# Kernel optimization log

Hardware: AMD Instinct MI355X
Metric: run time of the kernel (lower is better)

Reference implementation:

```python
import jax, jax.numpy as jnp
import numpy as np

TD_MAX = 1024  # matches init_kwargs td_max; ensemble_average=True


def setup_inputs() -> dict:
    key = jax.random.key(0)
    # trajectory: [T_frames, N_particles, 3]
    x = jax.random.normal(key, (4096, 2048, 3), dtype=jnp.float32)
    return {"x": x}


def reference(x):
    # Original (ensemble_average=True):
    #   MSD[td] = (1/n_t0) * sum_{t0=0}^{n_t0-1} mean_{n,d} (x[t0+td] - x[t0])^2
    # Since every t0 window has the same (N,3) size, this equals a single
    # mean over (t0, n, d) per lag td. We scan over lags to avoid
    # materializing the full [td_max, n_t0, N, 3] gather.
    T = x.shape[0]
    n_t0 = T - TD_MAX
    base = x[:n_t0]  # [n_t0, N, 3] shared origin frames

    def per_lag(carry, td):
        win = jax.lax.dynamic_slice_in_dim(x, td, n_t0, axis=0)  # [n_t0, N, 3]
        d = win - base
        return carry, jnp.mean(d * d)

    _, msd = jax.lax.scan(per_lag, None, jnp.arange(TD_MAX))
    return msd  # [td_max]
```

## Files before the change

kernel.cpp:

```cpp
#include <hip/hip_runtime.h>
#include <stdint.h>

#define T_TOTAL 4096
#define NT0     3072
#define CH      6144
#define TD_MAXL 1024

#define KS     4
#define KC     (CH / KS)
#define BK     32
#define NSTEP  (KC / BK)
#define NTI    24
#define ND     9
#define NTILE  (NTI * ND)
#define NBLK   (NTILE * KS)
#define LDHF   40

typedef _Float16 half8 __attribute__((ext_vector_type(8)));
typedef float    f32x4 __attribute__((ext_vector_type(4)));


__device__ inline void gload16(const void* g, void* l) {
    __builtin_amdgcn_global_load_lds(
        (const __attribute__((address_space(1))) unsigned int*)g,
        (__attribute__((address_space(3))) unsigned int*)l, 16, 0, 0);
}

__global__ __launch_bounds__(256) void s_kernel(const float* __restrict__ x,
                                                float* __restrict__ S,
                                                float* __restrict__ C) {
    const int t = blockIdx.x;
    if (t < TD_MAXL && threadIdx.x == 0) C[t] = 0.0f;
    const float4* row = (const float4*)(x + (size_t)t * CH);
    float s = 0.f;
    for (int k = threadIdx.x; k < CH / 4; k += 256) {
        float4 v = row[k];
        s = fmaf(v.x, v.x, s); s = fmaf(v.y, v.y, s);
        s = fmaf(v.z, v.z, s); s = fmaf(v.w, v.w, s);
    }
    #pragma unroll
    for (int off = 32; off >= 1; off >>= 1) s += __shfl_xor(s, off, 64);
    __shared__ float part[4];
    const int lane = threadIdx.x & 63, wid = threadIdx.x >> 6;
    if (lane == 0) part[wid] = s;
    __syncthreads();
    if (threadIdx.x == 0) S[t] = part[0] + part[1] + part[2] + part[3];
}

__device__ inline half8 pack8(const float4 u, const float4 v) {
    half8 h;
    h[0] = (_Float16)u.x; h[1] = (_Float16)u.y; h[2] = (_Float16)u.z; h[3] = (_Float16)u.w;
    h[4] = (_Float16)v.x; h[5] = (_Float16)v.y; h[6] = (_Float16)v.z; h[7] = (_Float16)v.w;
    return h;
}

__global__ __launch_bounds__(256) void cvt_kernel(const float* __restrict__ x,
                                                  _Float16* __restrict__ xh) {
    const size_t total = (size_t)T_TOTAL * CH;
    size_t i = ((size_t)blockIdx.x * 256 + threadIdx.x) * 8;
    const size_t stride = (size_t)gridDim.x * 256 * 8;
    for (; i < total; i += stride) {
        float4 u = *(const float4*)(x + i);
        float4 v = *(const float4*)(x + i + 4);
        *(half8*)(xh + i) = pack8(u, v);
    }
}

__global__ __launch_bounds__(256, 4) void cross_mfma(const _Float16* __restrict__ xh,
                                                     float* __restrict__ C) {
    __shared__ _Float16 As[2][128][BK];
    __shared__ _Float16 Bs[2][128][BK];
    __shared__ float    C_loc[256];

    const int tid = threadIdx.x;
    const int bid = blockIdx.x;
    const int xcd  = bid & 7;
    const int slot = bid >> 3;
    const int ks   = slot / 27;
    const int tt   = slot % 27;
    const int tile = xcd * 27 + tt;
    const int I    = tile / ND;
    const int D    = tile % ND;
    const int i0 = I * 128, j0 = (I + D) * 128;
    const int k0 = ks * KC;

    C_loc[tid] = 0.f;

    const int lane = tid & 63, wid = tid >> 6;

    const int rsub  = lane >> 2;
    const int pslot = lane & 3;
    const int swz   = ((pslot ^ (rsub & 3)) << 3);
    const int c0row = wid * 32;
    const _Float16* sA0 = xh + (size_t)(i0 + c0row + rsub) * CH + k0 + swz;
    const _Float16* sB0 = xh + (size_t)(j0 + c0row + rsub) * CH + k0 + swz;

#define STAGE(buf, toff) { \
        const size_t ko = (size_t)(toff) * BK; \
        gload16(sA0 + ko,            &As[buf][c0row][0]);      \
        gload16(sA0 + 16 * CH + ko,  &As[buf][c0row + 16][0]); \
        gload16(sB0 + ko,            &Bs[buf][c0row][0]);      \
        gload16(sB0 + 16 * CH + ko,  &Bs[buf][c0row + 16][0]); \
    }

    const int wm = wid >> 1, wn = wid & 1;
    const int fr = lane & 15, ss = lane >> 4;
    const int rdslot = ((ss ^ (fr & 3)) << 4);
    const int offA = (wm * 64 + fr) * 64 + rdslot;
    const int offB = (wn * 64 + fr) * 64 + rdslot;

    f32x4 acc[4][4];
    #pragma unroll
    for (int m = 0; m < 4; ++m)
        #pragma unroll
        for (int n = 0; n < 4; ++n) acc[m][n] = (f32x4)0.f;

    STAGE(0, 0);
    __syncthreads();

    int cur = 0;
    for (int t = 0; t < NSTEP; ++t) {
        if (t + 1 < NSTEP) STAGE(cur ^ 1, t + 1);

        const char* bA = (const char*)&As[cur][0][0];
        const char* bB = (const char*)&Bs[cur][0][0];
        half8 fA[4], fB[4];
        #pragma unroll
        for (int m = 0; m < 4; ++m)
            fA[m] = *(const half8*)(bA + offA + m * (16 * BK * 2));
        #pragma unroll
        for (int n = 0; n < 4; ++n)
            fB[n] = *(const half8*)(bB + offB + n * (16 * BK * 2));
        #pragma unroll
        for (int m = 0; m < 4; ++m)
            #pragma unroll
            for (int n = 0; n < 4; ++n)
                acc[m][n] = __builtin_amdgcn_mfma_f32_16x16x32_f16(fA[m], fB[n],
                                                                   acc[m][n], 0, 0, 0);
        __syncthreads();
        cur ^= 1;
    }
#undef STAGE

    float buck[7][4];
    #pragma unroll
    for (int dd = 0; dd < 7; ++dd)
        #pragma unroll
        for (int rr = 0; rr < 4; ++rr) buck[dd][rr] = 0.f;
    #pragma unroll
    for (int m = 0; m < 4; ++m)
        #pragma unroll
        for (int n = 0; n < 4; ++n)
            #pragma unroll
            for (int rr = 0; rr < 4; ++rr)
                buck[n - m + 3][rr] += acc[m][n][rr];

    const int obase = 64 * (wn - wm) + 128 + (fr - (ss << 2));
    #pragma unroll
    for (int dd = 0; dd < 7; ++dd)
        #pragma unroll
        for (int rr = 0; rr < 4; ++rr)
            atomicAdd(&C_loc[obase + 16 * (dd - 3) - rr], buck[dd][rr]);
    __syncthreads();

    const int td = D * 128 + tid - 128;
    if (td >= 0 && td < TD_MAXL) atomicAdd(&C[td], C_loc[tid]);
}

__global__ __launch_bounds__(256, 2) void cross_fallback(const float* __restrict__ x,
                                                         float* __restrict__ C) {
    __shared__ _Float16 As[2][128][LDHF];
    __shared__ _Float16 Bs[2][128][LDHF];
    __shared__ float    C_loc[256];
    const int tid = threadIdx.x;
    const int bid = blockIdx.x;
    const int xcd  = bid & 7;
    const int slot = bid >> 3;
    const int ks   = slot / 27;
    const int tt   = slot % 27;
    const int tile = xcd * 27 + tt;
    const int I    = tile / ND;
    const int D    = tile % ND;
    const int i0 = I * 128, j0 = (I + D) * 128;
    const int k0 = ks * KC;
    C_loc[tid] = 0.f;
    const int srow = tid >> 1, skq = (tid & 1) << 4;
    const float* gA = x + (size_t)(i0 + srow) * CH + k0 + skq;
    const float* gB = x + (size_t)(j0 + srow) * CH + k0 + skq;
    const int lane = tid & 63, wid = tid >> 6;
    const int wm = wid >> 1, wn = wid & 1;
    const int fr = lane & 15, ss = lane >> 4;
    const int rowA = wm * 64 + fr, rowB = wn * 64 + fr;
    f32x4 acc[4][4];
    #pragma unroll
    for (int m = 0; m < 4; ++m)
        #pragma unroll
        for (int n = 0; n < 4; ++n) acc[m][n] = (f32x4)0.f;
    {
        float4 a[4], b[4];
        #pragma unroll
        for (int q = 0; q < 4; ++q) { a[q] = ((const float4*)gA)[q]; b[q] = ((const float4*)gB)[q]; }
        *(half8*)&As[0][srow][skq]     = pack8(a[0], a[1]);
        *(half8*)&As[0][srow][skq + 8] = pack8(a[2], a[3]);
        *(half8*)&Bs[0][srow][skq]     = pack8(b[0], b[1]);
        *(half8*)&Bs[0][srow][skq + 8] = pack8(b[2], b[3]);
    }
    int cur = 0;
    for (int t = 0; t < NSTEP; ++t) {
        __syncthreads();
        float4 a[4], b[4];
        const bool more = (t + 1 < NSTEP);
        if (more) {
            const float* pA = gA + (size_t)(t + 1) * BK;
            const float* pB = gB + (size_t)(t + 1) * BK;
            #pragma unroll
            for (int q = 0; q < 4; ++q) { a[q] = ((const float4*)pA)[q]; b[q] = ((const float4*)pB)[q]; }
        }
        half8 fA[4], fB[4];
        #pragma unroll
        for (int m = 0; m < 4; ++m) fA[m] = *(const half8*)&As[cur][rowA + 16 * m][ss * 8];
        #pragma unroll
        for (int n = 0; n < 4; ++n) fB[n] = *(const half8*)&Bs[cur][rowB + 16 * n][ss * 8];
        #pragma unroll
        for (int m = 0; m < 4; ++m)
            #pragma unroll
            for (int n = 0; n < 4; ++n)
                acc[m][n] = __builtin_amdgcn_mfma_f32_16x16x32_f16(fA[m], fB[n], acc[m][n], 0, 0, 0);
        if (more) {
            const int nb = cur ^ 1;
            *(half8*)&As[nb][srow][skq]     = pack8(a[0], a[1]);
            *(half8*)&As[nb][srow][skq + 8] = pack8(a[2], a[3]);
            *(half8*)&Bs[nb][srow][skq]     = pack8(b[0], b[1]);
            *(half8*)&Bs[nb][srow][skq + 8] = pack8(b[2], b[3]);
        }
        cur ^= 1;
    }
    float buck[7][4];
    #pragma unroll
    for (int dd = 0; dd < 7; ++dd)
        #pragma unroll
        for (int rr = 0; rr < 4; ++rr) buck[dd][rr] = 0.f;
    #pragma unroll
    for (int m = 0; m < 4; ++m)
        #pragma unroll
        for (int n = 0; n < 4; ++n)
            #pragma unroll
            for (int rr = 0; rr < 4; ++rr)
                buck[n - m + 3][rr] += acc[m][n][rr];
    const int obase = 64 * (wn - wm) + 128 + (fr - (ss << 2));
    #pragma unroll
    for (int dd = 0; dd < 7; ++dd)
        #pragma unroll
        for (int rr = 0; rr < 4; ++rr)
            atomicAdd(&C_loc[obase + 16 * (dd - 3) - rr], buck[dd][rr]);
    __syncthreads();
    const int td = D * 128 + tid - 128;
    if (td >= 0 && td < TD_MAXL) atomicAdd(&C[td], C_loc[tid]);
}

__global__ __launch_bounds__(256) void combine_kernel(const float* __restrict__ S,
                                                      const float* __restrict__ C,
                                                      float* __restrict__ out) {
    const int td = blockIdx.x;
    float p = 0.f, q = 0.f;
    for (int t = threadIdx.x; t < NT0; t += 256) {
        p += S[t + td];
        q += S[t];
    }
    #pragma unroll
    for (int off = 32; off >= 1; off >>= 1) {
        p += __shfl_xor(p, off, 64);
        q += __shfl_xor(q, off, 64);
    }
    __shared__ float pp[4], qq[4];
    const int lane = threadIdx.x & 63, wid = threadIdx.x >> 6;
    if (lane == 0) { pp[wid] = p; qq[wid] = q; }
    __syncthreads();
    if (threadIdx.x == 0) {
        const float P = pp[0] + pp[1] + pp[2] + pp[3];
        const float Q = qq[0] + qq[1] + qq[2] + qq[3];
        const float inv_M = 1.0f / ((float)NT0 * (float)CH);
        out[td] = (P + Q - 2.0f * C[td]) * inv_M;
    }
}

extern "C" void kernel_launch(void* const* d_in, const int* in_sizes, int n_in,
                              void* d_out, int out_size, void* d_ws, size_t ws_size,
                              hipStream_t stream) {
    const float* x = (const float*)d_in[0];
    float* out = (float*)d_out;
    float* S = (float*)d_ws;
    float* C = (float*)((char*)d_ws + 16384);
    _Float16* xh = (_Float16*)((char*)d_ws + 32768);
    const size_t need = 32768 + (size_t)T_TOTAL * CH * sizeof(_Float16);

    s_kernel<<<dim3(T_TOTAL), dim3(256), 0, stream>>>(x, S, C);
    if (ws_size >= need) {
        cvt_kernel<<<dim3(12288), dim3(256), 0, stream>>>(x, xh);
        cross_mfma<<<dim3(NBLK), dim3(256), 0, stream>>>(xh, C);
    } else {
        cross_fallback<<<dim3(NBLK), dim3(256), 0, stream>>>(x, C);
    }
    combine_kernel<<<dim3(TD_MAXL), dim3(256), 0, stream>>>(S, C, out);
}
```

Baseline: 261.1 us.

## Fuse norm and fp16 conversion, enlarge cross-correlation tiles to 256x256

Merges the row-norm kernel and the fp16 conversion kernel into one prep kernel, so the fp32 trajectory is read once instead of twice. Replaces the 128x128 MFMA tile with a 256x256 tile using 512 threads, 8x4 accumulators per wave and a split-K of 8, which raises arithmetic intensity per LDS load. The cost is fewer banded tiles, more wasted work past the lag limit, higher register pressure and different occupancy. The fallback path now also runs the prep kernel, which writes to xh even though the workspace was too small.

```diff
diff --git a/kernel.cpp b/kernel.cpp
--- a/kernel.cpp
+++ b/kernel.cpp
@@ -6,14 +6,18 @@
 #define CH      6144
 #define TD_MAXL 1024
 
-#define KS     4
-#define KC     (CH / KS)
+#define KS2    8
+#define KC2    (CH / KS2)
 #define BK     32
-#define NSTEP  (KC / BK)
-#define NTI    24
-#define ND     9
-#define NTILE  (NTI * ND)
-#define NBLK   (NTILE * KS)
+#define NSTEP2 (KC2 / BK)
+#define NI2    12
+#define ND2    5
+#define NBLK2  (NI2 * ND2 * KS2)
+
+#define KSF    4
+#define KCF    (CH / KSF)
+#define NSTEPF (KCF / BK)
+#define NDF    9
 #define LDHF   40
 
 typedef _Float16 half8 __attribute__((ext_vector_type(8)));
@@ -24,27 +28,6 @@
     __builtin_amdgcn_global_load_lds(
         (const __attribute__((address_space(1))) unsigned int*)g,
         (__attribute__((address_space(3))) unsigned int*)l, 16, 0, 0);
-}
-
-__global__ __launch_bounds__(256) void s_kernel(const float* __restrict__ x,
-                                                float* __restrict__ S,
-                                                float* __restrict__ C) {
-    const int t = blockIdx.x;
-    if (t < TD_MAXL && threadIdx.x == 0) C[t] = 0.0f;
-    const float4* row = (const float4*)(x + (size_t)t * CH);
-    float s = 0.f;
-    for (int k = threadIdx.x; k < CH / 4; k += 256) {
-        float4 v = row[k];
-        s = fmaf(v.x, v.x, s); s = fmaf(v.y, v.y, s);
-        s = fmaf(v.z, v.z, s); s = fmaf(v.w, v.w, s);
-    }
-    #pragma unroll
-    for (int off = 32; off >= 1; off >>= 1) s += __shfl_xor(s, off, 64);
-    __shared__ float part[4];
-    const int lane = threadIdx.x & 63, wid = threadIdx.x >> 6;
-    if (lane == 0) part[wid] = s;
-    __syncthreads();
-    if (threadIdx.x == 0) S[t] = part[0] + part[1] + part[2] + part[3];
 }
 
 __device__ inline half8 pack8(const float4 u, const float4 v) {
@@ -54,64 +37,74 @@
     return h;
 }
 
-__global__ __launch_bounds__(256) void cvt_kernel(const float* __restrict__ x,
-                                                  _Float16* __restrict__ xh) {
-    const size_t total = (size_t)T_TOTAL * CH;
-    size_t i = ((size_t)blockIdx.x * 256 + threadIdx.x) * 8;
-    const size_t stride = (size_t)gridDim.x * 256 * 8;
-    for (; i < total; i += stride) {
-        float4 u = *(const float4*)(x + i);
-        float4 v = *(const float4*)(x + i + 4);
-        *(half8*)(xh + i) = pack8(u, v);
-    }
-}
-
-__global__ __launch_bounds__(256, 4) void cross_mfma(const _Float16* __restrict__ xh,
-                                                     float* __restrict__ C) {
-    __shared__ _Float16 As[2][128][BK];
-    __shared__ _Float16 Bs[2][128][BK];
-    __shared__ float    C_loc[256];
+__global__ __launch_bounds__(256) void prep_kernel(const float* __restrict__ x,
+                                                   _Float16* __restrict__ xh,
+                                                   float* __restrict__ S,
+                                                   float* __restrict__ C) {
+    const int t = blockIdx.x;
+    if (t < TD_MAXL && threadIdx.x == 0) C[t] = 0.0f;
+    const float4* row = (const float4*)(x + (size_t)t * CH);
+    _Float16* orow = xh + (size_t)t * CH;
+    float s = 0.f;
+    for (int k = threadIdx.x; k < CH / 8; k += 256) {
+        float4 u = row[2 * k], v = row[2 * k + 1];
+        s = fmaf(u.x, u.x, s); s = fmaf(u.y, u.y, s);
+        s = fmaf(u.z, u.z, s); s = fmaf(u.w, u.w, s);
+        s = fmaf(v.x, v.x, s); s = fmaf(v.y, v.y, s);
+        s = fmaf(v.z, v.z, s); s = fmaf(v.w, v.w, s);
+        *(half8*)(orow + 8 * k) = pack8(u, v);
+    }
+    #pragma unroll
+    for (int off = 32; off >= 1; off >>= 1) s += __shfl_xor(s, off, 64);
+    __shared__ float part[4];
+    const int lane = threadIdx.x & 63, wid = threadIdx.x >> 6;
+    if (lane == 0) part[wid] = s;
+    __syncthreads();
+    if (threadIdx.x == 0) S[t] = part[0] + part[1] + part[2] + part[3];
+}
+
+__global__ __launch_bounds__(512, 2) void cross_mfma2(const _Float16* __restrict__ xh,
+                                                      float* __restrict__ C) {
+    __shared__ _Float16 Ps[2][2][256][BK];
+    __shared__ float    C_loc[512];
 
     const int tid = threadIdx.x;
     const int bid = blockIdx.x;
-    const int xcd  = bid & 7;
+    const int ks   = bid & 7;
     const int slot = bid >> 3;
-    const int ks   = slot / 27;
-    const int tt   = slot % 27;
-    const int tile = xcd * 27 + tt;
-    const int I    = tile / ND;
-    const int D    = tile % ND;
-    const int i0 = I * 128, j0 = (I + D) * 128;
-    const int k0 = ks * KC;
-
-    C_loc[tid] = 0.f;
+    const int I    = slot / ND2;
+    const int D    = slot % ND2;
+    const int i0 = I * 256, j0 = (I + D) * 256;
+    const int k0 = ks * KC2;
+
+    if (tid < 512) C_loc[tid] = 0.f;
 
     const int lane = tid & 63, wid = tid >> 6;
 
-    const int rsub  = lane >> 2;
-    const int pslot = lane & 3;
-    const int swz   = ((pslot ^ (rsub & 3)) << 3);
-    const int c0row = wid * 32;
-    const _Float16* sA0 = xh + (size_t)(i0 + c0row + rsub) * CH + k0 + swz;
-    const _Float16* sB0 = xh + (size_t)(j0 + c0row + rsub) * CH + k0 + swz;
-
-#define STAGE(buf, toff) { \
-        const size_t ko = (size_t)(toff) * BK; \
-        gload16(sA0 + ko,            &As[buf][c0row][0]);      \
-        gload16(sA0 + 16 * CH + ko,  &As[buf][c0row + 16][0]); \
-        gload16(sB0 + ko,            &Bs[buf][c0row][0]);      \
-        gload16(sB0 + 16 * CH + ko,  &Bs[buf][c0row + 16][0]); \
-    }
-
-    const int wm = wid >> 1, wn = wid & 1;
+    const int isB  = wid >> 2;
+    const int wq   = wid & 3;
+    const int rsub = lane >> 2;
+    const int pslot= lane & 3;
+    const int swz  = (pslot ^ (rsub & 3)) << 3;
+    const _Float16* src0 = xh
+        + (size_t)((isB ? j0 : i0) + wq * 64 + rsub) * CH + k0 + swz;
+
+#define STAGE(buf, t) { \
+        gload16(src0 + (size_t)(t) * BK,               &Ps[buf][isB][wq * 64][0]);      \
+        gload16(src0 + (size_t)(t) * BK + 16 * CH,     &Ps[buf][isB][wq * 64 + 16][0]); \
+        gload16(src0 + (size_t)(t) * BK + 32 * CH,     &Ps[buf][isB][wq * 64 + 32][0]); \
+        gload16(src0 + (size_t)(t) * BK + 48 * CH,     &Ps[buf][isB][wq * 64 + 48][0]); \
+    }
+
+    const int wm = wid >> 2, wn = wid & 3;
     const int fr = lane & 15, ss = lane >> 4;
-    const int rdslot = ((ss ^ (fr & 3)) << 4);
-    const int offA = (wm * 64 + fr) * 64 + rdslot;
-    const int offB = (wn * 64 + fr) * 64 + rdslot;
-
-    f32x4 acc[4][4];
-    #pragma unroll
-    for (int m = 0; m < 4; ++m)
+    const int rdslot = (ss ^ (fr & 3)) << 4;
+    const int offA = (wm * 128 + fr) * (BK * 2) + rdslot;
+    const int offB = (wn * 64 + fr) * (BK * 2) + rdslot;
+
+    f32x4 acc[8][4];
+    #pragma unroll
+    for (int m = 0; m < 8; ++m)
         #pragma unroll
         for (int n = 0; n < 4; ++n) acc[m][n] = (f32x4)0.f;
 
@@ -119,20 +112,20 @@
     __syncthreads();
 
     int cur = 0;
-    for (int t = 0; t < NSTEP; ++t) {
-        if (t + 1 < NSTEP) STAGE(cur ^ 1, t + 1);
-
-        const char* bA = (const char*)&As[cur][0][0];
-        const char* bB = (const char*)&Bs[cur][0][0];
-        half8 fA[4], fB[4];
-        #pragma unroll
-        for (int m = 0; m < 4; ++m)
+    for (int t = 0; t < NSTEP2; ++t) {
+        if (t + 1 < NSTEP2) STAGE(cur ^ 1, t + 1);
+
+        const char* bA = (const char*)&Ps[cur][0][0][0];
+        const char* bB = (const char*)&Ps[cur][1][0][0];
+        half8 fA[8], fB[4];
+        #pragma unroll
+        for (int m = 0; m < 8; ++m)
             fA[m] = *(const half8*)(bA + offA + m * (16 * BK * 2));
         #pragma unroll
         for (int n = 0; n < 4; ++n)
             fB[n] = *(const half8*)(bB + offB + n * (16 * BK * 2));
         #pragma unroll
-        for (int m = 0; m < 4; ++m)
+        for (int m = 0; m < 8; ++m)
             #pragma unroll
             for (int n = 0; n < 4; ++n)
                 acc[m][n] = __builtin_amdgcn_mfma_f32_16x16x32_f16(fA[m], fB[n],
@@ -142,29 +135,31 @@
     }
 #undef STAGE
 
-    float buck[7][4];
-    #pragma unroll
-    for (int dd = 0; dd < 7; ++dd)
+    float buck[11][4];
+    #pragma unroll
+    for (int dd = 0; dd < 11; ++dd)
         #pragma unroll
         for (int rr = 0; rr < 4; ++rr) buck[dd][rr] = 0.f;
     #pragma unroll
-    for (int m = 0; m < 4; ++m)
+    for (int m = 0; m < 8; ++m)
         #pragma unroll
         for (int n = 0; n < 4; ++n)
             #pragma unroll
             for (int rr = 0; rr < 4; ++rr)
-                buck[n - m + 3][rr] += acc[m][n][rr];
-
-    const int obase = 64 * (wn - wm) + 128 + (fr - (ss << 2));
-    #pragma unroll
-    for (int dd = 0; dd < 7; ++dd)
+                buck[n - m + 7][rr] += acc[m][n][rr];
+
+    const int obase = 64 * wn - 128 * wm + 255 + (fr - (ss << 2));
+    #pragma unroll
+    for (int dd = 0; dd < 11; ++dd)
         #pragma unroll
         for (int rr = 0; rr < 4; ++rr)
-            atomicAdd(&C_loc[obase + 16 * (dd - 3) - rr], buck[dd][rr]);
-    __syncthreads();
-
-    const int td = D * 128 + tid - 128;
-    if (td >= 0 && td < TD_MAXL) atomicAdd(&C[td], C_loc[tid]);
+            atomicAdd(&C_loc[obase + 16 * (dd - 7) - rr], buck[dd][rr]);
+    __syncthreads();
+
+    if (tid < 511) {
+        const int td = D * 256 + tid - 255;
+        if (td >= 0 && td < TD_MAXL) atomicAdd(&C[td], C_loc[tid]);
+    }
 }
 
 __global__ __launch_bounds__(256, 2) void cross_fallback(const float* __restrict__ x,
@@ -179,10 +174,10 @@
     const int ks   = slot / 27;
     const int tt   = slot % 27;
     const int tile = xcd * 27 + tt;
-    const int I    = tile / ND;
-    const int D    = tile % ND;
+    const int I    = tile / NDF;
+    const int D    = tile % NDF;
     const int i0 = I * 128, j0 = (I + D) * 128;
-    const int k0 = ks * KC;
+    const int k0 = ks * KCF;
     C_loc[tid] = 0.f;
     const int srow = tid >> 1, skq = (tid & 1) << 4;
     const float* gA = x + (size_t)(i0 + srow) * CH + k0 + skq;
@@ -206,10 +201,10 @@
         *(half8*)&Bs[0][srow][skq + 8] = pack8(b[2], b[3]);
     }
     int cur = 0;
-    for (int t = 0; t < NSTEP; ++t) {
+    for (int t = 0; t < NSTEPF; ++t) {
         __syncthreads();
         float4 a[4], b[4];
-        const bool more = (t + 1 < NSTEP);
+        const bool more = (t + 1 < NSTEPF);
         if (more) {
             const float* pA = gA + (size_t)(t + 1) * BK;
             const float* pB = gB + (size_t)(t + 1) * BK;
@@ -294,12 +289,12 @@
     _Float16* xh = (_Float16*)((char*)d_ws + 32768);
     const size_t need = 32768 + (size_t)T_TOTAL * CH * sizeof(_Float16);
 
-    s_kernel<<<dim3(T_TOTAL), dim3(256), 0, stream>>>(x, S, C);
     if (ws_size >= need) {
-        cvt_kernel<<<dim3(12288), dim3(256), 0, stream>>>(x, xh);
-        cross_mfma<<<dim3(NBLK), dim3(256), 0, stream>>>(xh, C);
+        prep_kernel<<<dim3(T_TOTAL), dim3(256), 0, stream>>>(x, xh, S, C);
+        cross_mfma2<<<dim3(NBLK2), dim3(512), 0, stream>>>(xh, C);
     } else {
-        cross_fallback<<<dim3(NBLK), dim3(256), 0, stream>>>(x, C);
+        prep_kernel<<<dim3(T_TOTAL), dim3(256), 0, stream>>>(x, xh, S, C);
+        cross_fallback<<<dim3(216 * KSF), dim3(256), 0, stream>>>(x, C);
     }
     combine_kernel<<<dim3(TD_MAXL), dim3(256), 0, stream>>>(S, C, out);
 }
```

New measurement: 268.5 us. 1.03x slower.
